# Optimization experiments

Measured on AMD Instinct MI355X. Metric: run time of the kernel, lower is better.

## Reference

```python
import jax, jax.numpy as jnp
import numpy as np

TYPE_NUM = 40000
REL_NUM = 10000
N = TYPE_NUM + REL_NUM  # 50000 nodes
E = 800000              # edges (avg degree 16)
EMB, MID, OUT = 256, 256, 128


def setup_inputs() -> dict:
    key = jax.random.key(0)
    k0, k1, k2, k3 = jax.random.split(key, 4)
    # xavier-ish scales
    node_emb = jax.random.normal(k0, (N, EMB), jnp.float32) * (1.0 / np.sqrt(EMB))
    W1 = jax.random.normal(k1, (EMB, MID), jnp.float32) * (1.0 / np.sqrt(EMB))
    W2 = jax.random.normal(k2, (MID, OUT), jnp.float32) * (1.0 / np.sqrt(MID))
    b1 = jnp.zeros((MID,), jnp.float32)
    b2 = jnp.zeros((OUT,), jnp.float32)
    edge_index = jax.random.randint(k3, (2, E), 0, N, jnp.int32)
    return {"node_emb": node_emb, "W1": W1, "b1": b1, "W2": W2, "b2": b2,
            "edge_index": edge_index}


def _gcn_conv(X, W, b, src, dst):
    """torch_geometric GCNConv: x' = D^-1/2 (A+I) D^-1/2 (X W) + b."""
    n = X.shape[0]
    loop = jnp.arange(n, dtype=src.dtype)
    s = jnp.concatenate([src, loop])  # source j
    d = jnp.concatenate([dst, loop])  # target i
    deg = jax.ops.segment_sum(jnp.ones_like(d, dtype=X.dtype), d, num_segments=n)
    dis = jnp.where(deg > 0, jax.lax.rsqrt(deg), 0.0)
    h = X @ W                               # [n, out]
    norm = (dis[s] * dis[d])[:, None]       # [E+n, 1]
    msg = h[s] * norm                       # gather messages
    return jax.ops.segment_sum(msg, d, num_segments=n) + b


def reference(node_emb, W1, b1, W2, b2, edge_index):
    src, dst = edge_index[0], edge_index[1]
    # torch nn.GELU default is exact (erf) gelu
    X = jax.nn.gelu(_gcn_conv(node_emb, W1, b1, src, dst), approximate=False)
    X = jax.nn.gelu(_gcn_conv(X, W2, b2, src, dst), approximate=False)
    return X[:TYPE_NUM], X[TYPE_NUM:]
```

## Files before the change

kernel.cpp:

```cpp
#include <hip/hip_runtime.h>
#include <math.h>

#define EMB 256
#define MID 256
#define OUTF 128
#define KDIM 256
#define LDK 40

using frag_ab = __attribute__((ext_vector_type(8))) short;
using frag_cd = __attribute__((ext_vector_type(4))) float;
typedef float f32x2 __attribute__((ext_vector_type(2)));

__device__ __forceinline__ float gelu_exact(float x) {
    return 0.5f * x * (1.0f + erff(x * 0.70710678118654752f));
}

__device__ __forceinline__ unsigned short f2bf(float f) {
    union { float f; unsigned int i; } v;
    v.f = f;
    unsigned int r = v.i + 0x7fff + ((v.i >> 16) & 1);
    return (unsigned short)(r >> 16);
}

__device__ __forceinline__ f32x2 bfpair(unsigned int u) {
    union { unsigned int i; float f; } a, b;
    a.i = u << 16;
    b.i = u & 0xffff0000u;
    f32x2 r;
    r.x = a.f; r.y = b.f;
    return r;
}


__global__ void deg_kernel(const int* __restrict__ dst, int* __restrict__ deg, int E) {
    int e = blockIdx.x * blockDim.x + threadIdx.x;
    if (e < E) atomicAdd(&deg[dst[e]], 1);
}

__global__ __launch_bounds__(256) void scan_reduce(const int* __restrict__ deg,
                                                   int* __restrict__ partial, int n) {
    __shared__ int s[256];
    int i = blockIdx.x * 256 + threadIdx.x;
    s[threadIdx.x] = (i < n) ? deg[i] : 0;
    __syncthreads();
    for (int o = 128; o > 0; o >>= 1) {
        if (threadIdx.x < o) s[threadIdx.x] += s[threadIdx.x + o];
        __syncthreads();
    }
    if (threadIdx.x == 0) partial[blockIdx.x] = s[0];
}

__global__ __launch_bounds__(256) void scan_partials(int* __restrict__ partial, int nb) {
    __shared__ int s[256];
    int tid = threadIdx.x;
    int v = (tid < nb) ? partial[tid] : 0;
    s[tid] = v;
    __syncthreads();
    for (int o = 1; o < 256; o <<= 1) {
        int t = (tid >= o) ? s[tid - o] : 0;
        __syncthreads();
        s[tid] += t;
        __syncthreads();
    }
    if (tid < nb) partial[tid] = s[tid] - v;
}

__global__ __launch_bounds__(256) void scan_final(const int* __restrict__ deg,
                                                  const int* __restrict__ partial,
                                                  int* __restrict__ row_start,
                                                  int* __restrict__ cursor,
                                                  float* __restrict__ dis, int n, int E) {
    __shared__ int s[256];
    int tid = threadIdx.x;
    int i = blockIdx.x * 256 + tid;
    int v = (i < n) ? deg[i] : 0;
    s[tid] = v;
    __syncthreads();
    for (int o = 1; o < 256; o <<= 1) {
        int t = (tid >= o) ? s[tid - o] : 0;
        __syncthreads();
        s[tid] += t;
        __syncthreads();
    }
    int ex = s[tid] - v + partial[blockIdx.x];
    if (i < n) {
        row_start[i] = ex;
        cursor[i] = ex;
        dis[i] = rsqrtf((float)(v + 1));
    }
    if (i == 0) row_start[n] = E;
}

__global__ void fill_kernel(const int* __restrict__ src, const int* __restrict__ dst,
                            int* __restrict__ cursor, int* __restrict__ csr_src, int E) {
    int e = blockIdx.x * blockDim.x + threadIdx.x;
    if (e < E) {
        int d = dst[e];
        int p = atomicAdd(&cursor[d], 1);
        csr_src[p] = src[e];
    }
}

__global__ void wt_both(const float* __restrict__ W1, const float* __restrict__ W2,
                        unsigned short* __restrict__ W1t, unsigned short* __restrict__ W2t) {
    int id = blockIdx.x * blockDim.x + threadIdx.x;
    const int t1 = EMB * MID;
    if (id < t1) {
        int k = id >> 8, n = id & 255;
        W1t[(size_t)n * EMB + k] = f2bf(W1[(size_t)k * MID + n]);
    } else {
        id -= t1;
        if (id < MID * OUTF) {
            int k = id >> 7, n = id & 127;
            W2t[(size_t)n * MID + k] = f2bf(W2[(size_t)k * OUTF + n]);
        }
    }
}


template <bool A_FP32, int NT>
__global__ __launch_bounds__(256, 1) void mfma_gemm(const void* __restrict__ Av,
                                                    const unsigned short* __restrict__ Wt,
                                                    const float* __restrict__ dis,
                                                    unsigned short* __restrict__ C,
                                                    int M) {
    constexpr int Ntot = NT * 128;
    __shared__ __align__(16) unsigned short As[128 * LDK];
    __shared__ __align__(16) unsigned short Bs[NT * 128 * LDK];

    const int tid = threadIdx.x;
    const int m0 = blockIdx.x * 128;
    const int wave = tid >> 6, lane = tid & 63;
    const int wrow = (wave >> 1) * 64, wcol = (wave & 1) * 64;
    const int q = lane >> 4, r = lane & 15;

    frag_cd acc[NT][4][4] = {};

    const int qb = tid & 3;
    const int nb = tid >> 2;

    for (int ks = 0; ks < KDIM; ks += 32) {
        if (A_FP32) {
            const float* A = (const float*)Av;
            int qa = tid & 7;
            int ra = tid >> 3;
#pragma unroll
            for (int rr = 0; rr < 4; ++rr) {
                int row = ra + rr * 32;
                int grow = m0 + row;
                if (grow >= M) grow = M - 1;
                float4 v = *(const float4*)(A + (size_t)grow * KDIM + ks + qa * 4);
                ushort4 w;
                w.x = f2bf(v.x); w.y = f2bf(v.y); w.z = f2bf(v.z); w.w = f2bf(v.w);
                *(ushort4*)&As[row * LDK + qa * 4] = w;
            }
        } else {
            const unsigned short* A = (const unsigned short*)Av;
#pragma unroll
            for (int rr = 0; rr < 2; ++rr) {
                int row = nb + rr * 64;
                int grow = m0 + row;
                if (grow >= M) grow = M - 1;
                uint4 v = *(const uint4*)(A + (size_t)grow * KDIM + ks + qb * 8);
                *(uint4*)&As[row * LDK + qb * 8] = v;
            }
        }
#pragma unroll
        for (int rr = 0; rr < 2 * NT; ++rr) {
            int n = nb + rr * 64;
            uint4 v = *(const uint4*)(Wt + (size_t)n * KDIM + ks + qb * 8);
            *(uint4*)&Bs[n * LDK + qb * 8] = v;
        }
        __syncthreads();

        frag_ab af[4];
#pragma unroll
        for (int i = 0; i < 4; ++i)
            af[i] = *(const frag_ab*)&As[(wrow + i * 16 + r) * LDK + q * 8];
#pragma unroll
        for (int nt = 0; nt < NT; ++nt) {
            frag_ab bfr[4];
#pragma unroll
            for (int j = 0; j < 4; ++j)
                bfr[j] = *(const frag_ab*)&Bs[(nt * 128 + wcol + j * 16 + r) * LDK + q * 8];
#pragma unroll
            for (int i = 0; i < 4; ++i)
#pragma unroll
                for (int j = 0; j < 4; ++j)
                    acc[nt][i][j] = __builtin_amdgcn_mfma_f32_16x16x32_bf16(
                        af[i], bfr[j], acc[nt][i][j], 0, 0, 0);
        }
        __syncthreads();
    }

#pragma unroll
    for (int i = 0; i < 4; ++i)
#pragma unroll
        for (int g = 0; g < 4; ++g) {
            int row = m0 + wrow + i * 16 + q * 4 + g;
            if (row < M) {
                float sc = dis[row];
#pragma unroll
                for (int nt = 0; nt < NT; ++nt)
#pragma unroll
                    for (int j = 0; j < 4; ++j) {
                        int col = nt * 128 + wcol + j * 16 + r;
                        C[(size_t)row * Ntot + col] = f2bf(acc[nt][i][j][g] * sc);
                    }
            }
        }
}


template <int VEC> struct ldt;
template <> struct ldt<4> { using T = uint2; };
template <> struct ldt<2> { using T = unsigned int; };

template <int F, bool OUT_BF>
__global__ __launch_bounds__(256) void agg_gelu2(const unsigned short* __restrict__ h,
                                                 const float* __restrict__ dis,
                                                 const int* __restrict__ row_start,
                                                 const int* __restrict__ csr_src,
                                                 const float* __restrict__ bias,
                                                 void* __restrict__ out, int n) {
    constexpr int VEC = F / 64;
    using LT = typename ldt<VEC>::T;
    int wid = (blockIdx.x * 256 + threadIdx.x) >> 6;
    int lane = threadIdx.x & 63;
    if (wid >= n) return;
    const int c0 = lane * VEC;
    const unsigned short* hb = h + c0;

    f32x2 acc[VEC / 2];
    {
        LT s = *(const LT*)(hb + (size_t)wid * F);
        if (VEC == 4) {
            uint2 u = *(uint2*)&s;
            acc[0] = bfpair(u.x);
            acc[VEC / 2 - 1] = bfpair(u.y);
        } else {
            acc[0] = bfpair(*(unsigned int*)&s);
        }
    }

    int e0 = row_start[wid], e1 = row_start[wid + 1];
    for (int base = e0; base < e1; base += 64) {
        int rem = e1 - base;
        int m = rem < 64 ? rem : 64;
        int jmine = (lane < m) ? csr_src[base + lane] : n;
        int mp = (m + 7) & ~7;

        LT A[8], B[8];
        auto load8 = [&](LT* buf, int t) {
#pragma unroll
            for (int u = 0; u < 8; ++u) {
                int j = __builtin_amdgcn_readlane(jmine, t + u);
                buf[u] = *(const LT*)(hb + (size_t)j * F);
            }
        };
        auto acc8 = [&](const LT* buf) {
#pragma unroll
            for (int u = 0; u < 8; ++u) {
                if (VEC == 4) {
                    uint2 v = *(uint2*)&buf[u];
                    acc[0] += bfpair(v.x);
                    acc[VEC / 2 - 1] += bfpair(v.y);
                } else {
                    acc[0] += bfpair(*(unsigned int*)&buf[u]);
                }
            }
        };

        load8(A, 0);
        int t = 8;
        for (;;) {
            if (t >= mp) { acc8(A); break; }
            load8(B, t); acc8(A); t += 8;
            if (t >= mp) { acc8(B); break; }
            load8(A, t); acc8(B); t += 8;
        }
    }

    float di = dis[wid];
    float res[VEC];
#pragma unroll
    for (int p = 0; p < VEC / 2; ++p) {
        res[2 * p + 0] = gelu_exact(di * acc[p].x + bias[c0 + 2 * p + 0]);
        res[2 * p + 1] = gelu_exact(di * acc[p].y + bias[c0 + 2 * p + 1]);
    }

    if (OUT_BF) {
        unsigned short* ob = (unsigned short*)out + (size_t)wid * F + c0;
        if (VEC == 4) {
            uint2 pk;
            pk.x = (unsigned int)f2bf(res[0]) | ((unsigned int)f2bf(res[1]) << 16);
            pk.y = (unsigned int)f2bf(res[2]) | ((unsigned int)f2bf(res[3]) << 16);
            *(uint2*)ob = pk;
        } else {
            unsigned int pk = (unsigned int)f2bf(res[0]) | ((unsigned int)f2bf(res[1]) << 16);
            *(unsigned int*)ob = pk;
        }
    } else {
        float* ob = (float*)out + (size_t)wid * F + c0;
        if (VEC == 4) {
            float4 rv; rv.x = res[0]; rv.y = res[1]; rv.z = res[2]; rv.w = res[3];
            *(float4*)ob = rv;
        } else {
            float2 rv; rv.x = res[0]; rv.y = res[1];
            *(float2*)ob = rv;
        }
    }
}


extern "C" void kernel_launch(void* const* d_in, const int* in_sizes, int n_in,
                              void* d_out, int out_size, void* d_ws, size_t ws_size,
                              hipStream_t stream) {
    const float* node_emb = (const float*)d_in[0];
    const float* W1 = (const float*)d_in[1];
    const float* b1 = (const float*)d_in[2];
    const float* W2 = (const float*)d_in[3];
    const float* b2 = (const float*)d_in[4];
    const int* edge_index = (const int*)d_in[5];

    const int N = in_sizes[0] / EMB;
    const int E = in_sizes[5] / 2;
    const int* src = edge_index;
    const int* dst = edge_index + E;

    char* ws = (char*)d_ws;
    size_t off = 0;
    auto alloc = [&](size_t bytes) -> void* {
        off = (off + 255) & ~(size_t)255;
        void* p = ws + off;
        off += bytes;
        return p;
    };

    const int nb = (N + 255) / 256;

    int* deg = (int*)alloc((size_t)N * 4);
    int* row_start = (int*)alloc((size_t)(N + 1) * 4);
    int* cursor = (int*)alloc((size_t)N * 4);
    float* dis = (float*)alloc((size_t)N * 4);
    int* partial = (int*)alloc((size_t)nb * 4);
    int* csr_src = (int*)alloc((size_t)E * 4);
    unsigned short* W1t = (unsigned short*)alloc((size_t)EMB * MID * 2);
    unsigned short* W2t = (unsigned short*)alloc((size_t)MID * OUTF * 2);
    unsigned short* h1 = (unsigned short*)alloc((size_t)(N + 1) * MID * 2);
    unsigned short* X1 = (unsigned short*)alloc((size_t)N * MID * 2);
    unsigned short* h2 = h1;

    hipMemsetAsync(deg, 0, (size_t)N * 4, stream);
    deg_kernel<<<(E + 255) / 256, 256, 0, stream>>>(dst, deg, E);
    scan_reduce<<<nb, 256, 0, stream>>>(deg, partial, N);
    scan_partials<<<1, 256, 0, stream>>>(partial, nb);
    scan_final<<<nb, 256, 0, stream>>>(deg, partial, row_start, cursor, dis, N, E);
    fill_kernel<<<(E + 255) / 256, 256, 0, stream>>>(src, dst, cursor, csr_src, E);
    wt_both<<<(EMB * MID + MID * OUTF + 255) / 256, 256, 0, stream>>>(W1, W2, W1t, W2t);

    const int gm = (N + 127) / 128;

    hipMemsetAsync(h1 + (size_t)N * MID, 0, MID * 2, stream);

    mfma_gemm<true, 2><<<gm, 256, 0, stream>>>(node_emb, W1t, dis, h1, N);
    agg_gelu2<256, true><<<(N + 3) / 4, 256, 0, stream>>>(h1, dis, row_start, csr_src,
                                                          b1, X1, N);

    mfma_gemm<false, 1><<<gm, 256, 0, stream>>>(X1, W2t, dis, h2, N);
    hipMemsetAsync(h2 + (size_t)N * OUTF, 0, OUTF * 2, stream);
    agg_gelu2<128, false><<<(N + 3) / 4, 256, 0, stream>>>(h2, dis, row_start, csr_src,
                                                           b2, d_out, N);
}
```

Before: 323.2 us.

## Fuse setup kernels and split aggregation wave into half-waves with wider loads

```diff
diff --git a/kernel.cpp b/kernel.cpp
--- a/kernel.cpp
+++ b/kernel.cpp
@@ -37,58 +37,58 @@
     if (e < E) atomicAdd(&deg[dst[e]], 1);
 }
 
-__global__ __launch_bounds__(256) void scan_reduce(const int* __restrict__ deg,
-                                                   int* __restrict__ partial, int n) {
-    __shared__ int s[256];
-    int i = blockIdx.x * 256 + threadIdx.x;
-    s[threadIdx.x] = (i < n) ? deg[i] : 0;
+#define WB1 (EMB * MID / 1024)
+#define WB2 (MID * OUTF / 1024)
+__global__ __launch_bounds__(1024) void setup_kernel(
+    const float* __restrict__ W1, const float* __restrict__ W2,
+    unsigned short* __restrict__ W1t, unsigned short* __restrict__ W2t,
+    const int* __restrict__ deg, int* __restrict__ row_start, int* __restrict__ cursor,
+    float* __restrict__ dis, unsigned short* __restrict__ h1pad,
+    unsigned short* __restrict__ h2pad, int n, int E) {
+    int b = blockIdx.x;
+    int tid = threadIdx.x;
+    if (b < WB1) {
+        int id = b * 1024 + tid;
+        int k = id >> 8, nn = id & 255;
+        W1t[(size_t)nn * EMB + k] = f2bf(W1[(size_t)k * MID + nn]);
+        return;
+    }
+    b -= WB1;
+    if (b < WB2) {
+        int id = b * 1024 + tid;
+        int k = id >> 7, nn = id & 127;
+        W2t[(size_t)nn * MID + k] = f2bf(W2[(size_t)k * OUTF + nn]);
+        return;
+    }
+    b -= WB2;
+    if (b == 0) {
+        if (tid < MID) h1pad[tid] = 0;
+        else if (tid < MID + OUTF) h2pad[tid - MID] = 0;
+        return;
+    }
+    __shared__ int sp[1024];
+    int per = (n + 1023) >> 10;
+    int s0 = tid * per;
+    int s1 = s0 + per; if (s1 > n) s1 = n;
+    int sum = 0;
+    for (int i = s0; i < s1; ++i) sum += deg[i];
+    sp[tid] = sum;
     __syncthreads();
-    for (int o = 128; o > 0; o >>= 1) {
-        if (threadIdx.x < o) s[threadIdx.x] += s[threadIdx.x + o];
+    for (int o = 1; o < 1024; o <<= 1) {
+        int t = (tid >= o) ? sp[tid - o] : 0;
         __syncthreads();
-    }
-    if (threadIdx.x == 0) partial[blockIdx.x] = s[0];
-}
-
-__global__ __launch_bounds__(256) void scan_partials(int* __restrict__ partial, int nb) {
-    __shared__ int s[256];
-    int tid = threadIdx.x;
-    int v = (tid < nb) ? partial[tid] : 0;
-    s[tid] = v;
-    __syncthreads();
-    for (int o = 1; o < 256; o <<= 1) {
-        int t = (tid >= o) ? s[tid - o] : 0;
+        sp[tid] += t;
         __syncthreads();
-        s[tid] += t;
-        __syncthreads();
-    }
-    if (tid < nb) partial[tid] = s[tid] - v;
-}
-
-__global__ __launch_bounds__(256) void scan_final(const int* __restrict__ deg,
-                                                  const int* __restrict__ partial,
-                                                  int* __restrict__ row_start,
-                                                  int* __restrict__ cursor,
-                                                  float* __restrict__ dis, int n, int E) {
-    __shared__ int s[256];
-    int tid = threadIdx.x;
-    int i = blockIdx.x * 256 + tid;
-    int v = (i < n) ? deg[i] : 0;
-    s[tid] = v;
-    __syncthreads();
-    for (int o = 1; o < 256; o <<= 1) {
-        int t = (tid >= o) ? s[tid - o] : 0;
-        __syncthreads();
-        s[tid] += t;
-        __syncthreads();
-    }
-    int ex = s[tid] - v + partial[blockIdx.x];
-    if (i < n) {
-        row_start[i] = ex;
-        cursor[i] = ex;
-        dis[i] = rsqrtf((float)(v + 1));
-    }
-    if (i == 0) row_start[n] = E;
+    }
+    int run = sp[tid] - sum;
+    for (int i = s0; i < s1; ++i) {
+        int d = deg[i];
+        row_start[i] = run;
+        cursor[i] = run;
+        dis[i] = rsqrtf((float)(d + 1));
+        run += d;
+    }
+    if (tid == 0) row_start[n] = E;
 }
 
 __global__ void fill_kernel(const int* __restrict__ src, const int* __restrict__ dst,
@@ -98,22 +98,6 @@
         int d = dst[e];
         int p = atomicAdd(&cursor[d], 1);
         csr_src[p] = src[e];
-    }
-}
-
-__global__ void wt_both(const float* __restrict__ W1, const float* __restrict__ W2,
-                        unsigned short* __restrict__ W1t, unsigned short* __restrict__ W2t) {
-    int id = blockIdx.x * blockDim.x + threadIdx.x;
-    const int t1 = EMB * MID;
-    if (id < t1) {
-        int k = id >> 8, n = id & 255;
-        W1t[(size_t)n * EMB + k] = f2bf(W1[(size_t)k * MID + n]);
-    } else {
-        id -= t1;
-        if (id < MID * OUTF) {
-            int k = id >> 7, n = id & 127;
-            W2t[(size_t)n * MID + k] = f2bf(W2[(size_t)k * OUTF + n]);
-        }
     }
 }
 
@@ -212,35 +196,33 @@
 }
 
 
-template <int VEC> struct ldt;
-template <> struct ldt<4> { using T = uint2; };
-template <> struct ldt<2> { using T = unsigned int; };
+template <int PER> struct ldt2;
+template <> struct ldt2<8> { using T = uint4; };
+template <> struct ldt2<4> { using T = uint2; };
 
 template <int F, bool OUT_BF>
-__global__ __launch_bounds__(256) void agg_gelu2(const unsigned short* __restrict__ h,
+__global__ __launch_bounds__(256) void agg_gelu3(const unsigned short* __restrict__ h,
                                                  const float* __restrict__ dis,
                                                  const int* __restrict__ row_start,
                                                  const int* __restrict__ csr_src,
                                                  const float* __restrict__ bias,
                                                  void* __restrict__ out, int n) {
-    constexpr int VEC = F / 64;
-    using LT = typename ldt<VEC>::T;
+    constexpr int PER = F / 32;
+    using LT = typename ldt2<PER>::T;
     int wid = (blockIdx.x * 256 + threadIdx.x) >> 6;
     int lane = threadIdx.x & 63;
     if (wid >= n) return;
-    const int c0 = lane * VEC;
+    const int half = lane >> 5;
+    const int c0 = (lane & 31) * PER;
     const unsigned short* hb = h + c0;
 
-    f32x2 acc[VEC / 2];
+    f32x2 acc[PER / 2];
     {
         LT s = *(const LT*)(hb + (size_t)wid * F);
-        if (VEC == 4) {
-            uint2 u = *(uint2*)&s;
-            acc[0] = bfpair(u.x);
-            acc[VEC / 2 - 1] = bfpair(u.y);
-        } else {
-            acc[0] = bfpair(*(unsigned int*)&s);
-        }
+        float m0 = half ? 0.0f : 1.0f;
+        const unsigned int* u = (const unsigned int*)&s;
+#pragma unroll
+        for (int p = 0; p < PER / 2; ++p) acc[p] = bfpair(u[p]) * m0;
     }
 
     int e0 = row_start[wid], e1 = row_start[wid + 1];
@@ -250,64 +232,66 @@
         int jmine = (lane < m) ? csr_src[base + lane] : n;
         int mp = (m + 7) & ~7;
 
-        LT A[8], B[8];
-        auto load8 = [&](LT* buf, int t) {
-#pragma unroll
-            for (int u = 0; u < 8; ++u) {
-                int j = __builtin_amdgcn_readlane(jmine, t + u);
+        LT A[4], B[4];
+        auto load4 = [&](LT* buf, int t) {
+#pragma unroll
+            for (int u = 0; u < 4; ++u) {
+                int ja = __builtin_amdgcn_readlane(jmine, t + 2 * u);
+                int jb = __builtin_amdgcn_readlane(jmine, t + 2 * u + 1);
+                int j = half ? jb : ja;
                 buf[u] = *(const LT*)(hb + (size_t)j * F);
             }
         };
-        auto acc8 = [&](const LT* buf) {
-#pragma unroll
-            for (int u = 0; u < 8; ++u) {
-                if (VEC == 4) {
-                    uint2 v = *(uint2*)&buf[u];
-                    acc[0] += bfpair(v.x);
-                    acc[VEC / 2 - 1] += bfpair(v.y);
-                } else {
-                    acc[0] += bfpair(*(unsigned int*)&buf[u]);
-                }
+        auto acc4 = [&](const LT* buf) {
+#pragma unroll
+            for (int u = 0; u < 4; ++u) {
+                const unsigned int* w = (const unsigned int*)&buf[u];
+#pragma unroll
+                for (int p = 0; p < PER / 2; ++p) acc[p] += bfpair(w[p]);
             }
         };
 
-        load8(A, 0);
+        load4(A, 0);
         int t = 8;
         for (;;) {
-            if (t >= mp) { acc8(A); break; }
-            load8(B, t); acc8(A); t += 8;
-            if (t >= mp) { acc8(B); break; }
-            load8(A, t); acc8(B); t += 8;
-        }
-    }
-
-    float di = dis[wid];
-    float res[VEC];
-#pragma unroll
-    for (int p = 0; p < VEC / 2; ++p) {
-        res[2 * p + 0] = gelu_exact(di * acc[p].x + bias[c0 + 2 * p + 0]);
-        res[2 * p + 1] = gelu_exact(di * acc[p].y + bias[c0 + 2 * p + 1]);
-    }
-
-    if (OUT_BF) {
-        unsigned short* ob = (unsigned short*)out + (size_t)wid * F + c0;
-        if (VEC == 4) {
-            uint2 pk;
-            pk.x = (unsigned int)f2bf(res[0]) | ((unsigned int)f2bf(res[1]) << 16);
-            pk.y = (unsigned int)f2bf(res[2]) | ((unsigned int)f2bf(res[3]) << 16);
-            *(uint2*)ob = pk;
+            if (t >= mp) { acc4(A); break; }
+            load4(B, t); acc4(A); t += 8;
+            if (t >= mp) { acc4(B); break; }
+            load4(A, t); acc4(B); t += 8;
+        }
+    }
+
+#pragma unroll
+    for (int p = 0; p < PER / 2; ++p) {
+        acc[p].x += __shfl_xor(acc[p].x, 32);
+        acc[p].y += __shfl_xor(acc[p].y, 32);
+    }
+
+    if (half == 0) {
+        float di = dis[wid];
+        float res[PER];
+#pragma unroll
+        for (int p = 0; p < PER / 2; ++p) {
+            res[2 * p + 0] = gelu_exact(di * acc[p].x + bias[c0 + 2 * p + 0]);
+            res[2 * p + 1] = gelu_exact(di * acc[p].y + bias[c0 + 2 * p + 1]);
+        }
+        if (OUT_BF) {
+            unsigned int pk[PER / 2];
+#pragma unroll
+            for (int p = 0; p < PER / 2; ++p)
+                pk[p] = (unsigned int)f2bf(res[2 * p]) | ((unsigned int)f2bf(res[2 * p + 1]) << 16);
+            unsigned short* ob = (unsigned short*)out + (size_t)wid * F + c0;
+            if (PER == 8) *(uint4*)ob = *(uint4*)pk;
+            else *(uint2*)ob = *(uint2*)pk;
         } else {
-            unsigned int pk = (unsigned int)f2bf(res[0]) | ((unsigned int)f2bf(res[1]) << 16);
-            *(unsigned int*)ob = pk;
-        }
-    } else {
-        float* ob = (float*)out + (size_t)wid * F + c0;
-        if (VEC == 4) {
-            float4 rv; rv.x = res[0]; rv.y = res[1]; rv.z = res[2]; rv.w = res[3];
-            *(float4*)ob = rv;
-        } else {
-            float2 rv; rv.x = res[0]; rv.y = res[1];
-            *(float2*)ob = rv;
+            float* ob = (float*)out + (size_t)wid * F + c0;
+            if (PER == 4) {
+                float4 rv; rv.x = res[0]; rv.y = res[1]; rv.z = res[2]; rv.w = res[3];
+                *(float4*)ob = rv;
+            } else {
+#pragma unroll
+                for (int u = 0; u < PER; ++u) ob[u] = res[u];
+            }
         }
     }
 }
@@ -337,38 +321,30 @@
         return p;
     };
 
-    const int nb = (N + 255) / 256;
-
     int* deg = (int*)alloc((size_t)N * 4);
     int* row_start = (int*)alloc((size_t)(N + 1) * 4);
     int* cursor = (int*)alloc((size_t)N * 4);
     float* dis = (float*)alloc((size_t)N * 4);
-    int* partial = (int*)alloc((size_t)nb * 4);
     int* csr_src = (int*)alloc((size_t)E * 4);
     unsigned short* W1t = (unsigned short*)alloc((size_t)EMB * MID * 2);
     unsigned short* W2t = (unsigned short*)alloc((size_t)MID * OUTF * 2);
     unsigned short* h1 = (unsigned short*)alloc((size_t)(N + 1) * MID * 2);
+    unsigned short* h2 = (unsigned short*)alloc((size_t)(N + 1) * OUTF * 2);
     unsigned short* X1 = (unsigned short*)alloc((size_t)N * MID * 2);
-    unsigned short* h2 = h1;
 
     hipMemsetAsync(deg, 0, (size_t)N * 4, stream);
     deg_kernel<<<(E + 255) / 256, 256, 0, stream>>>(dst, deg, E);
-    scan_reduce<<<nb, 256, 0, stream>>>(deg, partial, N);
-    scan_partials<<<1, 256, 0, stream>>>(partial, nb);
-    scan_final<<<nb, 256, 0, stream>>>(deg, partial, row_start, cursor, dis, N, E);
+    setup_kernel<<<WB1 + WB2 + 2, 1024, 0, stream>>>(
+        W1, W2, W1t, W2t, deg, row_start, cursor, dis,
+        h1 + (size_t)N * MID, h2 + (size_t)N * OUTF, N, E);
     fill_kernel<<<(E + 255) / 256, 256, 0, stream>>>(src, dst, cursor, csr_src, E);
-    wt_both<<<(EMB * MID + MID * OUTF + 255) / 256, 256, 0, stream>>>(W1, W2, W1t, W2t);
 
     const int gm = (N + 127) / 128;
 
-    hipMemsetAsync(h1 + (size_t)N * MID, 0, MID * 2, stream);
-
     mfma_gemm<true, 2><<<gm, 256, 0, stream>>>(node_emb, W1t, dis, h1, N);
-    agg_gelu2<256, true><<<(N + 3) / 4, 256, 0, stream>>>(h1, dis, row_start, csr_src,
+    agg_gelu3<256, true><<<(N + 3) / 4, 256, 0, stream>>>(h1, dis, row_start, csr_src,
                                                           b1, X1, N);
-
     mfma_gemm<false, 1><<<gm, 256, 0, stream>>>(X1, W2t, dis, h2, N);
-    hipMemsetAsync(h2 + (size_t)N * OUTF, 0, OUTF * 2, stream);
-    agg_gelu2<128, false><<<(N + 3) / 4, 256, 0, stream>>>(h2, dis, row_start, csr_src,
+    agg_gelu3<128, false><<<(N + 3) / 4, 256, 0, stream>>>(h2, dis, row_start, csr_src,
                                                            b2, d_out, N);
 }
```

Measured after the change: 454.3 us. +40.5%, slower.
